# Kernel optimization log

Hardware: AMD Instinct MI355X
Metric: run time of the kernel (lower is better)

## Reference

```python
import jax, jax.numpy as jnp
import numpy as np

BATCH, NUM_FEAT, EMB = 1024, 32, 16
HIDDEN = [128, 128, 128]


def setup_inputs() -> dict:
    key = jax.random.key(0)
    ks = jax.random.split(key, 4)
    inputs = jax.random.normal(ks[0], (BATCH, NUM_FEAT, EMB), dtype=jnp.float32)
    # Conv1D kernel_size=1 -> dense weight of shape (in_dim, units) per layer.
    # in_dim_i = h_{i-1} * num_feat, with h_{-1} = num_feat.
    in0 = NUM_FEAT * NUM_FEAT          # 1024
    in1 = HIDDEN[0] * NUM_FEAT         # 4096
    in2 = HIDDEN[1] * NUM_FEAT         # 4096
    scale = lambda fan_in: (1.0 / np.sqrt(fan_in)).astype(np.float32) if isinstance(fan_in, np.ndarray) else np.float32(1.0 / np.sqrt(fan_in))
    W0 = jax.random.normal(ks[1], (in0, HIDDEN[0]), dtype=jnp.float32) * scale(in0)
    W1 = jax.random.normal(ks[2], (in1, HIDDEN[1]), dtype=jnp.float32) * scale(in1)
    W2 = jax.random.normal(ks[3], (in2, HIDDEN[2]), dtype=jnp.float32) * scale(in2)
    b0 = jnp.zeros((HIDDEN[0],), dtype=jnp.float32)
    b1 = jnp.zeros((HIDDEN[1],), dtype=jnp.float32)
    b2 = jnp.zeros((HIDDEN[2],), dtype=jnp.float32)
    return {"inputs": inputs, "W0": W0, "b0": b0, "W1": W1, "b1": b1, "W2": W2, "b2": b2}


def reference(inputs, W0, b0, W1, b1, W2, b2):
    # inputs: (b, m, e) -> x0: (b, e, m)  [channels-last like tf.transpose perm=[0,2,1]]
    x0 = jnp.transpose(inputs, (0, 2, 1))
    b, d, m = x0.shape
    params = [(W0, b0), (W1, b1), (W2, b2)]
    xl = x0
    layer_outs = []
    for i, (W, bias) in enumerate(params):
        h = xl.shape[-1]
        # outer product over feature axes: (b, d, h, m) -> flatten to (b, d, h*m)
        zl = jnp.einsum('bdh,bdm->bdhm', xl, x0).reshape(b, d, h * m)
        xl = zl @ W + bias  # 1x1 conv == per-position GEMM
        if i < len(params) - 1:
            xl = jax.nn.relu(xl)
        layer_outs.append(xl)
    # sum over embedding axis d, concat over layers -> (b, sum(HIDDEN))
    return jnp.concatenate([o.sum(axis=1) for o in layer_outs], axis=1)
```

## Files before the change

kernel.cpp:

```cpp
#include <hip/hip_runtime.h>


typedef unsigned int u32;
typedef __attribute__((ext_vector_type(8))) short short8;
typedef __attribute__((ext_vector_type(4))) float f32x4;
typedef __attribute__((ext_vector_type(4))) u32 u32x4;

#define R_TOTAL 16384
#define GLOBAL_AS __attribute__((address_space(1)))
#define LDS_AS __attribute__((address_space(3)))

union PackU { u32 u[4]; short8 s; };
union PackB { u32x4 v; short8 s; };

__device__ __forceinline__ u32 pack_rne(float a, float b) {
  u32 r;
  asm("v_cvt_pk_bf16_f32 %0, %1, %2" : "=v"(r) : "v"(a), "v"(b));
  return r;
}

__device__ __forceinline__ void build_x0t_body(const float* __restrict__ in,
                                               float* __restrict__ x0t,
                                               int bid, int tid, float* t) {
  const int b0 = bid * 8;
  #pragma unroll
  for (int rep = 0; rep < 4; ++rep) {
    int idx = tid + rep * 256;
    *(float4*)&t[idx * 4] = *(const float4*)&in[(size_t)b0 * 512 + idx * 4];
  }
  __syncthreads();
  #pragma unroll
  for (int rep = 0; rep < 4; ++rep) {
    int idx = tid + rep * 256;
    int m = idx >> 5, rem = idx & 31;
    int bl = rem >> 2, dq = rem & 3;
    *(float4*)&x0t[(size_t)m * R_TOTAL + (b0 + bl) * 16 + dq * 4] =
        *(const float4*)&t[bl * 512 + m * 16 + dq * 4];
  }
}

__device__ __forceinline__ void swizzle_body(const float* __restrict__ W,
                                             u32* __restrict__ wt,
                                             int bid, int tid, float* wl) {
  const int t = bid >> 2, nq = bid & 3;
  {
    int kk = tid >> 3, c4 = tid & 7;
    float4 v = *(const float4*)&W[(size_t)(t * 32 + kk) * 128 + nq * 32 + c4 * 4];
    wl[kk * 33 + c4 * 4 + 0] = v.x;
    wl[kk * 33 + c4 * 4 + 1] = v.y;
    wl[kk * 33 + c4 * 4 + 2] = v.z;
    wl[kk * 33 + c4 * 4 + 3] = v.w;
  }
  __syncthreads();
  if (tid < 128) {
    int nl = tid >> 2, p = tid & 3;
    int q = p ^ (nl & 3);
    u32 o[4];
    #pragma unroll
    for (int jj = 0; jj < 4; ++jj)
      o[jj] = pack_rne(wl[(q * 8 + 2 * jj + 0) * 33 + nl],
                       wl[(q * 8 + 2 * jj + 1) * 33 + nl]);
    *(u32x4*)(wt + (size_t)(t * 4 + nq) * 512 + nl * 16 + p * 4) =
        u32x4{o[0], o[1], o[2], o[3]};
  }
}

__global__ __launch_bounds__(256) void prep_all(
    const float* __restrict__ in, float* __restrict__ x0t,
    const float* __restrict__ W0, u32* __restrict__ wt0,
    const float* __restrict__ W1, u32* __restrict__ wt1,
    const float* __restrict__ W2, u32* __restrict__ wt2) {
  __shared__ float sh[4096];
  const int b = blockIdx.x, tid = threadIdx.x;
  if (b < 128)      build_x0t_body(in, x0t, b, tid, sh);
  else if (b < 256) swizzle_body(W0, wt0, b - 128, tid, sh);
  else if (b < 768) swizzle_body(W1, wt1, b - 256, tid, sh);
  else              swizzle_body(W2, wt2, b - 768, tid, sh);
}

__device__ __forceinline__ void stage2k(const u32* g, u32* l, int lane) {
  const GLOBAL_AS u32* gp = (const GLOBAL_AS u32*)g;
  LDS_AS u32* lp = (LDS_AS u32*)l;
  #pragma unroll
  for (int i = 0; i < 2; ++i)
    __builtin_amdgcn_global_load_lds(gp + i * 256 + lane * 4, lp + i * 256, 16, 0, 0);
}

#define SB() __builtin_amdgcn_sched_barrier(0)

#define KITER(I, SLOT, TOPVM, LGKM, DO_STAGE, READ_NEXT, BCUR, BNXT)           \
  {                                                                            \
    __builtin_amdgcn_s_waitcnt(TOPVM);                                         \
    SB();                                                                      \
    if (READ_NEXT) {                                                           \
      const u32* nbuf = mybuf + ((SLOT) ^ 1) * 512;                            \
      BNXT[0].v = *(const u32x4*)(nbuf + ln15 * 16 + ((q ^ sw) * 4));          \
      BNXT[1].v = *(const u32x4*)(nbuf + (16 + ln15) * 16 + ((q ^ sw) * 4));   \
    }                                                                          \
    SB();                                                                      \
    __builtin_amdgcn_s_waitcnt(LGKM);                                          \
    SB();                                                                      \
    if (DO_STAGE) {                                                            \
      stage2k(wt + (size_t)((t0 + (I) + 2) * 4 + nq) * 512,                    \
              mybuf + (SLOT) * 512, lane);                                     \
    }                                                                          \
    SB();                                                                      \
    __builtin_amdgcn_s_setprio(1);                                             \
    f32x4 Y0[4], Y1[4];                                                        \
    _Pragma("unroll")                                                          \
    for (int f = 0; f < 4; ++f)                                                \
      Y0[f] = __builtin_amdgcn_mfma_f32_16x16x32_bf16(Ah[f].s, BCUR[0].s, zero4, 0, 0, 0); \
    _Pragma("unroll")                                                          \
    for (int f = 0; f < 4; ++f)                                                \
      Y1[f] = __builtin_amdgcn_mfma_f32_16x16x32_bf16(Ah[f].s, BCUR[1].s, zero4, 0, 0, 0); \
    _Pragma("unroll")                                                          \
    for (int f = 0; f < 4; ++f) {                                              \
      acc[f][0] += xn[SLOT][f] * Y0[f];                                        \
      acc[f][1] += xn[SLOT][f] * Y1[f];                                        \
    }                                                                          \
    __builtin_amdgcn_s_setprio(0);                                             \
    SB();                                                                      \
    if (DO_STAGE) {                                                            \
      const float* xp = xt + (size_t)(t0 + (I) + 2) * R_TOTAL + r0;            \
      xn[SLOT][0] = *(const f32x4*)(xp + 0 + q * 4);                           \
      xn[SLOT][1] = *(const f32x4*)(xp + 16 + q * 4);                          \
      xn[SLOT][2] = *(const f32x4*)(xp + 32 + q * 4);                          \
      xn[SLOT][3] = *(const f32x4*)(xp + 48 + q * 4);                          \
    }                                                                          \
    SB();                                                                      \
  }

template <int NT, bool RELU, bool STORE_X>
__global__ __launch_bounds__(512, 2) void layer_mfma(
    const float* __restrict__ xt,
    const float* __restrict__ x0t,
    const u32* __restrict__ wt,
    const float* __restrict__ bias,
    float* __restrict__ xoutT,
    float* __restrict__ osum)
{
  constexpr int HT = NT / 2;
  static_assert((HT & 1) == 0 && HT >= 4, "pair-loop needs even HT >= 4");
  __shared__ u32 smem[16384];

  const int tid = threadIdx.x;
  const int w = tid >> 6, lane = tid & 63;
  const int ln15 = lane & 15, q = lane >> 4;
  const int kh = w & 1, nq = w >> 1;
  const int r0 = blockIdx.x * 64;
  const int sw = ln15 & 3;
  u32* mybuf = smem + w * 2048;

  PackU Ah[4];
  #pragma unroll
  for (int f = 0; f < 4; ++f) {
    const int rbase = r0 + f * 16 + ln15;
    float e[8];
    #pragma unroll
    for (int j = 0; j < 8; ++j) e[j] = x0t[(size_t)(q * 8 + j) * R_TOTAL + rbase];
    #pragma unroll
    for (int jj = 0; jj < 4; ++jj)
      Ah[f].u[jj] = pack_rne(e[2 * jj], e[2 * jj + 1]);
  }

  f32x4 acc[4][2];
  #pragma unroll
  for (int f = 0; f < 4; ++f)
    #pragma unroll
    for (int c = 0; c < 2; ++c) acc[f][c] = f32x4{0.f, 0.f, 0.f, 0.f};
  const f32x4 zero4 = {0.f, 0.f, 0.f, 0.f};

  const int t0 = kh * HT;

  f32x4 xn[2][4];
  stage2k(wt + (size_t)(t0 * 4 + nq) * 512, mybuf, lane);
  SB();
  {
    const float* xp = xt + (size_t)t0 * R_TOTAL + r0;
    xn[0][0] = *(const f32x4*)(xp + 0 + q * 4);
    xn[0][1] = *(const f32x4*)(xp + 16 + q * 4);
    xn[0][2] = *(const f32x4*)(xp + 32 + q * 4);
    xn[0][3] = *(const f32x4*)(xp + 48 + q * 4);
  }
  SB();
  stage2k(wt + (size_t)((t0 + 1) * 4 + nq) * 512, mybuf + 512, lane);
  SB();
  {
    const float* xp = xt + (size_t)(t0 + 1) * R_TOTAL + r0;
    xn[1][0] = *(const f32x4*)(xp + 0 + q * 4);
    xn[1][1] = *(const f32x4*)(xp + 16 + q * 4);
    xn[1][2] = *(const f32x4*)(xp + 32 + q * 4);
    xn[1][3] = *(const f32x4*)(xp + 48 + q * 4);
  }
  SB();
  __builtin_amdgcn_s_waitcnt(0x0F7A);
  SB();
  PackB ba[2], bb[2];
  {
    ba[0].v = *(const u32x4*)(mybuf + ln15 * 16 + ((q ^ sw) * 4));
    ba[1].v = *(const u32x4*)(mybuf + (16 + ln15) * 16 + ((q ^ sw) * 4));
  }
  SB();

  for (int i = 0; i < HT - 2; i += 2) {
    KITER(i,     0, 0x0F74, 0xC27F, 1, 1, ba, bb);
    KITER(i + 1, 1, 0x0F74, 0xC27F, 1, 1, bb, ba);
  }
  KITER(HT - 2, 0, 0x0F74, 0xC27F, 0, 1, ba, bb);
  KITER(HT - 1, 1, 0x0F70, 0xC07F, 0, 0, bb, ba);

  __syncthreads();
  if (kh == 1) {
    u32* reg = mybuf;
    #pragma unroll
    for (int f = 0; f < 4; ++f)
      #pragma unroll
      for (int c = 0; c < 2; ++c)
        *(f32x4*)(reg + ((size_t)(f * 2 + c) * 64 + lane) * 4) = acc[f][c];
  }
  __syncthreads();
  if (kh == 0) {
    const u32* reg = smem + (w + 1) * 2048;
    float bs[2];
    #pragma unroll
    for (int c = 0; c < 2; ++c) bs[c] = bias[nq * 32 + c * 16 + ln15];

    f32x4 vv[4][2];
    #pragma unroll
    for (int f = 0; f < 4; ++f) {
      #pragma unroll
      for (int c = 0; c < 2; ++c) {
        f32x4 part = *(const f32x4*)(reg + ((size_t)(f * 2 + c) * 64 + lane) * 4);
        f32x4 v = acc[f][c] + part;
        v.x += bs[c]; v.y += bs[c]; v.z += bs[c]; v.w += bs[c];
        if (RELU) {
          v.x = fmaxf(v.x, 0.f); v.y = fmaxf(v.y, 0.f);
          v.z = fmaxf(v.z, 0.f); v.w = fmaxf(v.w, 0.f);
        }
        vv[f][c] = v;
        float s = v.x + v.y + v.z + v.w;
        s += __shfl_xor(s, 16, 64);
        s += __shfl_xor(s, 32, 64);
        if (q == 0)
          osum[(size_t)((r0 >> 4) + f) * 384 + nq * 32 + c * 16 + ln15] = s;
      }
    }

    if (STORE_X) {
      u32* myreg = mybuf;
      #pragma unroll
      for (int f = 0; f < 4; ++f)
        #pragma unroll
        for (int c = 0; c < 2; ++c)
          *(f32x4*)(myreg + ((size_t)(f * 2 + c) * 64 + lane) * 4) = vv[f][c];
      #pragma unroll
      for (int c = 0; c < 2; ++c) {
        #pragma unroll
        for (int s = 0; s < 4; ++s) {
          f32x4 vr = *(const f32x4*)(myreg +
              ((size_t)(s * 2 + c) * 64 + (lane & 3) * 16 + (lane >> 2)) * 4);
          const int col = nq * 32 + c * 16 + (lane >> 2);
          *(f32x4*)&xoutT[(size_t)col * R_TOTAL + r0 + s * 16 + (lane & 3) * 4] = vr;
        }
      }
    }
  }
}

extern "C" void kernel_launch(void* const* d_in, const int* in_sizes, int n_in,
                              void* d_out, int out_size, void* d_ws, size_t ws_size,
                              hipStream_t stream) {
  const float* in = (const float*)d_in[0];
  const float* W0 = (const float*)d_in[1];
  const float* b0 = (const float*)d_in[2];
  const float* W1 = (const float*)d_in[3];
  const float* b1 = (const float*)d_in[4];
  const float* W2 = (const float*)d_in[5];
  const float* b2 = (const float*)d_in[6];
  float* out = (float*)d_out;

  float* X0T = (float*)d_ws;
  float* X1T = X0T + (size_t)32 * R_TOTAL;
  float* X2T = X1T + (size_t)128 * R_TOTAL;
  u32* Wt0 = (u32*)(X2T + (size_t)128 * R_TOTAL);
  u32* Wt1 = Wt0 + (size_t)32 * 4 * 512;
  u32* Wt2 = Wt1 + (size_t)128 * 4 * 512;

  prep_all<<<1280, 256, 0, stream>>>(in, X0T, W0, Wt0, W1, Wt1, W2, Wt2);

  layer_mfma<32, true, true><<<256, 512, 0, stream>>>(X0T, X0T, Wt0, b0, X1T, out + 0);
  layer_mfma<128, true, true><<<256, 512, 0, stream>>>(X1T, X0T, Wt1, b1, X2T, out + 128);
  layer_mfma<128, false, false><<<256, 512, 0, stream>>>(X2T, X0T, Wt2, b2, nullptr, out + 256);
}
```

Baseline: 137.2 us.

## Load swizzled weight fragments directly from global into registers, bypassing LDS

Replaces the global_load_lds staging of weight tiles into LDS followed by LDS reads with direct global vector loads into the MFMA B-operand registers. The weights are double-buffered in registers (ba/bb) and prefetched two iterations ahead, and the waitcnt values are adjusted to match the new count of outstanding loads. This removes the LDS round trip and the lgkm waits, but each wave now depends on global load latency per iteration and may use more registers.

```diff
diff --git a/kernel.cpp b/kernel.cpp
--- a/kernel.cpp
+++ b/kernel.cpp
@@ -7,8 +7,6 @@
 typedef __attribute__((ext_vector_type(4))) u32 u32x4;
 
 #define R_TOTAL 16384
-#define GLOBAL_AS __attribute__((address_space(1)))
-#define LDS_AS __attribute__((address_space(3)))
 
 union PackU { u32 u[4]; short8 s; };
 union PackB { u32x4 v; short8 s; };
@@ -78,41 +76,20 @@
   else              swizzle_body(W2, wt2, b - 768, tid, sh);
 }
 
-__device__ __forceinline__ void stage2k(const u32* g, u32* l, int lane) {
-  const GLOBAL_AS u32* gp = (const GLOBAL_AS u32*)g;
-  LDS_AS u32* lp = (LDS_AS u32*)l;
-  #pragma unroll
-  for (int i = 0; i < 2; ++i)
-    __builtin_amdgcn_global_load_lds(gp + i * 256 + lane * 4, lp + i * 256, 16, 0, 0);
-}
-
 #define SB() __builtin_amdgcn_sched_barrier(0)
 
-#define KITER(I, SLOT, TOPVM, LGKM, DO_STAGE, READ_NEXT, BCUR, BNXT)           \
+#define KITER(I, SLOT, TOPVM, DO_ISSUE, BP)                                    \
   {                                                                            \
     __builtin_amdgcn_s_waitcnt(TOPVM);                                         \
-    SB();                                                                      \
-    if (READ_NEXT) {                                                           \
-      const u32* nbuf = mybuf + ((SLOT) ^ 1) * 512;                            \
-      BNXT[0].v = *(const u32x4*)(nbuf + ln15 * 16 + ((q ^ sw) * 4));          \
-      BNXT[1].v = *(const u32x4*)(nbuf + (16 + ln15) * 16 + ((q ^ sw) * 4));   \
-    }                                                                          \
-    SB();                                                                      \
-    __builtin_amdgcn_s_waitcnt(LGKM);                                          \
-    SB();                                                                      \
-    if (DO_STAGE) {                                                            \
-      stage2k(wt + (size_t)((t0 + (I) + 2) * 4 + nq) * 512,                    \
-              mybuf + (SLOT) * 512, lane);                                     \
-    }                                                                          \
     SB();                                                                      \
     __builtin_amdgcn_s_setprio(1);                                             \
     f32x4 Y0[4], Y1[4];                                                        \
     _Pragma("unroll")                                                          \
     for (int f = 0; f < 4; ++f)                                                \
-      Y0[f] = __builtin_amdgcn_mfma_f32_16x16x32_bf16(Ah[f].s, BCUR[0].s, zero4, 0, 0, 0); \
+      Y0[f] = __builtin_amdgcn_mfma_f32_16x16x32_bf16(Ah[f].s, BP[0].s, zero4, 0, 0, 0); \
     _Pragma("unroll")                                                          \
     for (int f = 0; f < 4; ++f)                                                \
-      Y1[f] = __builtin_amdgcn_mfma_f32_16x16x32_bf16(Ah[f].s, BCUR[1].s, zero4, 0, 0, 0); \
+      Y1[f] = __builtin_amdgcn_mfma_f32_16x16x32_bf16(Ah[f].s, BP[1].s, zero4, 0, 0, 0); \
     _Pragma("unroll")                                                          \
     for (int f = 0; f < 4; ++f) {                                              \
       acc[f][0] += xn[SLOT][f] * Y0[f];                                        \
@@ -120,7 +97,10 @@
     }                                                                          \
     __builtin_amdgcn_s_setprio(0);                                             \
     SB();                                                                      \
-    if (DO_STAGE) {                                                            \
+    if (DO_ISSUE) {                                                            \
+      const u32* ib = wt + (size_t)((t0 + (I) + 2) * 4 + nq) * 512;            \
+      BP[0].v = *(const u32x4*)(ib + boff0);                                   \
+      BP[1].v = *(const u32x4*)(ib + boff1);                                   \
       const float* xp = xt + (size_t)(t0 + (I) + 2) * R_TOTAL + r0;            \
       xn[SLOT][0] = *(const f32x4*)(xp + 0 + q * 4);                           \
       xn[SLOT][1] = *(const f32x4*)(xp + 16 + q * 4);                          \
@@ -151,6 +131,9 @@
   const int sw = ln15 & 3;
   u32* mybuf = smem + w * 2048;
 
+  const int boff0 = ln15 * 16 + ((q ^ sw) * 4);
+  const int boff1 = (16 + ln15) * 16 + ((q ^ sw) * 4);
+
   PackU Ah[4];
   #pragma unroll
   for (int f = 0; f < 4; ++f) {
@@ -172,10 +155,12 @@
 
   const int t0 = kh * HT;
 
+  PackB ba[2], bb[2];
   f32x4 xn[2][4];
-  stage2k(wt + (size_t)(t0 * 4 + nq) * 512, mybuf, lane);
-  SB();
   {
+    const u32* ib = wt + (size_t)(t0 * 4 + nq) * 512;
+    ba[0].v = *(const u32x4*)(ib + boff0);
+    ba[1].v = *(const u32x4*)(ib + boff1);
     const float* xp = xt + (size_t)t0 * R_TOTAL + r0;
     xn[0][0] = *(const f32x4*)(xp + 0 + q * 4);
     xn[0][1] = *(const f32x4*)(xp + 16 + q * 4);
@@ -183,9 +168,10 @@
     xn[0][3] = *(const f32x4*)(xp + 48 + q * 4);
   }
   SB();
-  stage2k(wt + (size_t)((t0 + 1) * 4 + nq) * 512, mybuf + 512, lane);
-  SB();
   {
+    const u32* ib = wt + (size_t)((t0 + 1) * 4 + nq) * 512;
+    bb[0].v = *(const u32x4*)(ib + boff0);
+    bb[1].v = *(const u32x4*)(ib + boff1);
     const float* xp = xt + (size_t)(t0 + 1) * R_TOTAL + r0;
     xn[1][0] = *(const f32x4*)(xp + 0 + q * 4);
     xn[1][1] = *(const f32x4*)(xp + 16 + q * 4);
@@ -193,21 +179,13 @@
     xn[1][3] = *(const f32x4*)(xp + 48 + q * 4);
   }
   SB();
-  __builtin_amdgcn_s_waitcnt(0x0F7A);
-  SB();
-  PackB ba[2], bb[2];
-  {
-    ba[0].v = *(const u32x4*)(mybuf + ln15 * 16 + ((q ^ sw) * 4));
-    ba[1].v = *(const u32x4*)(mybuf + (16 + ln15) * 16 + ((q ^ sw) * 4));
-  }
-  SB();
 
   for (int i = 0; i < HT - 2; i += 2) {
-    KITER(i,     0, 0x0F74, 0xC27F, 1, 1, ba, bb);
-    KITER(i + 1, 1, 0x0F74, 0xC27F, 1, 1, bb, ba);
-  }
-  KITER(HT - 2, 0, 0x0F74, 0xC27F, 0, 1, ba, bb);
-  KITER(HT - 1, 1, 0x0F70, 0xC07F, 0, 0, bb, ba);
+    KITER(i,     0, 0x0F76, 1, ba);
+    KITER(i + 1, 1, 0x0F76, 1, bb);
+  }
+  KITER(HT - 2, 0, 0x0F76, 0, ba);
+  KITER(HT - 1, 1, 0x0F70, 0, bb);
 
   __syncthreads();
   if (kh == 1) {
```

Result: no change. 136.4 us (-0.6%).
